# Kernel optimization log

Measured on AMD Instinct MI355X. Metric: run time of the kernel, lower is better.

Reference implementation:

```python
import jax, jax.numpy as jnp
import numpy as np

ALPHA = 16.0  # init kwarg alpha
K = 32        # init kwarg k: threshold = (K+1)-th smallest candidate pair
N, D = 4096, 128
NUM_CLASSES = 512


def setup_inputs() -> dict:
    key = jax.random.key(0)
    k1, k2 = jax.random.split(key)
    x = jax.random.normal(k1, (N, D), dtype=jnp.float32)
    # L2-normalize so self-similarity == 1 (the torch code's `pos_pair_ < 1`
    # filter relies on this to drop the self pair)
    inputs = x / jnp.linalg.norm(x, axis=1, keepdims=True)
    targets = jax.random.randint(k2, (N,), 0, NUM_CLASSES)
    return {"inputs": inputs, "targets": targets}


def reference(inputs, targets):
    sim = inputs @ inputs.T                       # [n, n]
    same = targets[:, None] == targets[None, :]   # [n, n]
    valid_pos = same & (sim < 1.0)                # pos pairs, self excluded
    valid_neg = ~same
    included = valid_pos | valid_neg              # union = torch's `pair`
    inf = jnp.float32(jnp.inf)

    # threshold = sorted(pair)[K] per row (K-th index, 0-based)
    masked = jnp.where(included, sim, inf)
    threshold = jnp.sort(masked, axis=1)[:, K]    # [n]

    base = jnp.mean(sim, axis=1, keepdims=True)   # [n, 1] torch: mean(sim_mat[i])
    w = jnp.exp(ALPHA * (base - sim))             # [n, n]

    below = sim < threshold[:, None]
    pos_sel = valid_pos & below
    neg_sel = valid_neg & below
    pos_sum = jnp.sum(jnp.where(pos_sel, w, 0.0), axis=1)  # [n]
    neg_sum = jnp.sum(jnp.where(neg_sel, w, 0.0), axis=1)  # [n]

    # fallback: if no pos pair below threshold, use the smallest pos similarity
    min_pos = jnp.min(jnp.where(valid_pos, sim, inf), axis=1)
    pos_fallback = jnp.exp(ALPHA * (base[:, 0] - min_pos))
    has_pos = jnp.any(pos_sel, axis=1)
    pos_logit = jnp.where(has_pos, pos_sum, pos_fallback)

    loss = jnp.mean(-jnp.log(pos_logit / (pos_logit + neg_sum)))

    # diagnostics from the LAST row (torch reads pos_pair_/neg_pair_ after loop)
    last = sim[-1]
    mean_pos_sim = jnp.sum(jnp.where(valid_pos[-1], last, 0.0)) / jnp.sum(valid_pos[-1])
    mean_neg_sim = jnp.sum(jnp.where(valid_neg[-1], last, 0.0)) / jnp.sum(valid_neg[-1])
    prec = jnp.float32(0.0)  # torch code: c stays 0
    return loss, prec, mean_pos_sim, mean_neg_sim
```

## Files before the change

kernel.cpp:

```cpp
#include <hip/hip_runtime.h>
#include <math.h>

#define NN 4096
#define DD 128
#define ALPHA_C 16.0f
#define KSEL 32
#define P2F -0.19f
#define SLOTS 16

typedef __attribute__((ext_vector_type(8))) short bf16x8;
typedef __attribute__((ext_vector_type(4))) float f32x4;

__device__ __forceinline__ unsigned f2k(float f) {
  unsigned b = __float_as_uint(f);
  return (b & 0x80000000u) ? ~b : (b | 0x80000000u);
}
__device__ __forceinline__ float k2f(unsigned k) {
  unsigned b = (k & 0x80000000u) ? (k & 0x7FFFFFFFu) : ~k;
  return __uint_as_float(b);
}

__device__ __forceinline__ double wsum_d(double v) {
  #pragma unroll
  for (int m = 32; m; m >>= 1) v += __shfl_xor(v, m, 64);
  return v;
}
__device__ __forceinline__ int wsum_i(int v) {
  #pragma unroll
  for (int m = 32; m; m >>= 1) v += __shfl_xor(v, m, 64);
  return v;
}
__device__ __forceinline__ float wsum_f(float v) {
  #pragma unroll
  for (int m = 32; m; m >>= 1) v += __shfl_xor(v, m, 64);
  return v;
}
__device__ __forceinline__ float wmin_f(float v) {
  #pragma unroll
  for (int m = 32; m; m >>= 1) v = fminf(v, __shfl_xor(v, m, 64));
  return v;
}

__global__ __launch_bounds__(256) void nca_prep(
    const float* __restrict__ x, short* __restrict__ xhi, short* __restrict__ xlo,
    double* __restrict__ selfdot, int* __restrict__ flag) {
  __shared__ double sd[16][16];

  const int tid = threadIdx.x;
  const int f  = blockIdx.x * 256 + tid;
  if (f == 0) flag[0] = 0;
  const int l  = f & 63;
  const int kb = (f >> 6) & 3;
  const int rg = f >> 8;
  const int rloc = l & 15;
  const int row = (rg << 4) + rloc;
  const int k0  = (kb << 5) + ((l >> 4) << 3);
  const float* src = x + (size_t)row * DD + k0;
  float4 v0 = *reinterpret_cast<const float4*>(src);
  float4 v1 = *reinterpret_cast<const float4*>(src + 4);
  float vv[8] = {v0.x, v0.y, v0.z, v0.w, v1.x, v1.y, v1.z, v1.w};
  bf16x8 h, lo;
  double sdp = 0.0;
  #pragma unroll
  for (int q = 0; q < 8; ++q) {
    sdp += (double)vv[q] * (double)vv[q];
    unsigned u  = __float_as_uint(vv[q]);
    unsigned hb = (u + 0x7FFFu + ((u >> 16) & 1u)) >> 16;
    float hf    = __uint_as_float(hb << 16);
    float lf    = vv[q] - hf;
    unsigned ul = __float_as_uint(lf);
    unsigned lb = (ul + 0x7FFFu + ((ul >> 16) & 1u)) >> 16;
    h[q] = (short)hb; lo[q] = (short)lb;
  }
  *reinterpret_cast<bf16x8*>(xhi + (size_t)f * 8) = h;
  *reinterpret_cast<bf16x8*>(xlo + (size_t)f * 8) = lo;

  sd[rloc][(tid >> 4)] = sdp;
  __syncthreads();
  if (tid < 16) {
    double s = 0.0;
    #pragma unroll
    for (int q = 0; q < 16; ++q) s += sd[tid][q];
    selfdot[(rg << 4) + tid] = s;
  }
}

__global__ __launch_bounds__(256) void nca_gemm(
    const short* __restrict__ xhi, const short* __restrict__ xlo,
    const int* __restrict__ tgt, uint2* __restrict__ winbuf,
    unsigned char* __restrict__ wcbuf, float* __restrict__ diagneg) {
  __shared__ int wcl[32];

  const int tid = threadIdx.x;
  const int w   = tid >> 6;
  const int l   = tid & 63;
  const int bid = blockIdx.x;
  const int swz = ((bid & 7) << 8) + (bid >> 3);
  const int rg  = swz >> 4;
  const int cg  = swz & 15;
  const int R   = rg << 5;
  const int C   = (cg << 8) + (w << 6);
  const int rga = rg << 1;
  const int rgb = (cg << 4) + (w << 2);

  if (tid < 32) wcl[tid] = 0;
  __syncthreads();

  f32x4 acc[2][4];
  #pragma unroll
  for (int rt = 0; rt < 2; ++rt)
    #pragma unroll
    for (int t = 0; t < 4; ++t) acc[rt][t] = (f32x4){0.f, 0.f, 0.f, 0.f};

  #pragma unroll
  for (int kb = 0; kb < 4; ++kb) {
    bf16x8 ah[2], al[2], bh[4], bl[4];
    #pragma unroll
    for (int rt = 0; rt < 2; ++rt) {
      const size_t off = ((size_t)((rga + rt) * 4 + kb) * 64 + l) * 8;
      ah[rt] = *reinterpret_cast<const bf16x8*>(xhi + off);
      al[rt] = *reinterpret_cast<const bf16x8*>(xlo + off);
    }
    #pragma unroll
    for (int t = 0; t < 4; ++t) {
      const size_t off = ((size_t)((rgb + t) * 4 + kb) * 64 + l) * 8;
      bh[t] = *reinterpret_cast<const bf16x8*>(xhi + off);
      bl[t] = *reinterpret_cast<const bf16x8*>(xlo + off);
    }
    #pragma unroll
    for (int rt = 0; rt < 2; ++rt)
      #pragma unroll
      for (int t = 0; t < 4; ++t) {
        acc[rt][t] = __builtin_amdgcn_mfma_f32_16x16x32_bf16(ah[rt], bh[t], acc[rt][t], 0, 0, 0);
        acc[rt][t] = __builtin_amdgcn_mfma_f32_16x16x32_bf16(ah[rt], bl[t], acc[rt][t], 0, 0, 0);
        acc[rt][t] = __builtin_amdgcn_mfma_f32_16x16x32_bf16(al[rt], bh[t], acc[rt][t], 0, 0, 0);
      }
  }

  const int rbase = (l >> 4) << 2;
  const int cc    = l & 15;
  const unsigned P2k = f2k(P2F);
  const bool diagblk = (R + 32 == NN);

  int tr[2][4], tc[4];
  #pragma unroll
  for (int rt = 0; rt < 2; ++rt)
    #pragma unroll
    for (int r = 0; r < 4; ++r) tr[rt][r] = tgt[R + (rt << 4) + rbase + r];
  #pragma unroll
  for (int t = 0; t < 4; ++t) tc[t] = tgt[C + (t << 4) + cc];

  #pragma unroll
  for (int rt = 0; rt < 2; ++rt) {
    #pragma unroll
    for (int r = 0; r < 4; ++r) {
      const int row_l = (rt << 4) + rbase + r;
      const int grow  = R + row_l;
      #pragma unroll
      for (int t = 0; t < 4; ++t) {
        const float s = acc[rt][t][r];
        const int j = C + (t << 4) + cc;
        const bool same = (tc[t] == tr[rt][r]);
        const unsigned key = f2k(s);
        const bool app = (j != grow) && (same || (key < P2k));
        if (app) {
          int slot = atomicAdd(&wcl[row_l], 1);
          if (slot < SLOTS)
            winbuf[(size_t)grow * 256 + (cg << 4) + slot] =
                make_uint2(key, same ? 1u : 0u);
        }
      }
    }
  }

  if (diagblk) {
    const int tN1 = tgt[NN - 1];
    float negs = 0.f;
    #pragma unroll
    for (int t = 0; t < 4; ++t)
      negs += (tc[t] != tN1) ? acc[1][t][3] : 0.f;
    negs = ((l >> 4) == 3) ? negs : 0.f;
    #pragma unroll
    for (int m = 1; m < 16; m <<= 1) negs += __shfl_xor(negs, m, 64);
    if (l == 48) diagneg[(cg << 2) + w] = negs;
  }

  __syncthreads();
  if (tid < 32) {
    int c = wcl[tid];
    wcbuf[(size_t)(R + tid) * 16 + cg] = (unsigned char)(c > 255 ? 255 : c);
  }
}

__global__ __launch_bounds__(256) void nca_combine(
    const double* __restrict__ selfdot, const int* __restrict__ tgt,
    const uint2* __restrict__ winbuf, const unsigned char* __restrict__ wcbuf,
    const float* __restrict__ diagneg, int* __restrict__ flag,
    float* __restrict__ row_loss, float* __restrict__ out) {
  const int tid = threadIdx.x, w = tid >> 6, lane = tid & 63;
  const int i = blockIdx.x * 4 + w;

  const double selfd = selfdot[i];
  const bool self_pos = (selfd < 1.0);

  const int wcq_l = (lane < 16) ? (int)wcbuf[(size_t)i * 16 + lane] : 0;
  const bool ovf = (__ballot(wcq_l > SLOTS) != 0ull);

  unsigned k[4]  = {0xFFFFFFFFu, 0xFFFFFFFFu, 0xFFFFFFFFu, 0xFFFFFFFFu};
  unsigned sm[4] = {0u, 0u, 0u, 0u};
  #pragma unroll
  for (int q = 0; q < 4; ++q) {
    const int sigma = (q << 6) + lane;
    const int wcq = __shfl(wcq_l, sigma >> 4, 64);
    if ((sigma & 15) < (wcq < SLOTS ? wcq : SLOTS)) {
      uint2 e = winbuf[(size_t)i * 256 + sigma];
      k[q] = e.x; sm[q] = e.y;
    }
  }

  const unsigned P2k = f2k(P2F);
  int c2 = 0;
  #pragma unroll
  for (int q = 0; q < 4; ++q) c2 += (int)__popcll(__ballot(k[q] < P2k));
  const bool fast = (c2 > KSEL) && (!ovf);
  if (!fast) {
    if (lane == 0) { int p = atomicAdd(&flag[0], 1); flag[1 + p] = i; }
    return;
  }

  unsigned thrkey = 0;
  for (int b = 31; b >= 0; --b) {
    unsigned mid = thrkey | (1u << b);
    int c = 0;
    #pragma unroll
    for (int q = 0; q < 4; ++q) c += (int)__popcll(__ballot(k[q] < mid));
    if (c <= KSEL) thrkey = mid;
  }

  float wp = 0.f, wn = 0.f, minp = __builtin_inff();
  int hp = 0;
  #pragma unroll
  for (int q = 0; q < 4; ++q) {
    const float s = k2f(k[q]);
    if (k[q] < thrkey) {
      float e = expf(-ALPHA_C * s);
      if (sm[q]) { wp += e; hp = 1; } else wn += e;
    }
    if (sm[q] && s < 1.0f) minp = fminf(minp, s);
  }
  wp = wsum_f(wp); wn = wsum_f(wn); hp = wsum_i(hp); minp = wmin_f(minp);

  const float minp2 = self_pos ? fminf(minp, (float)selfd) : minp;
  const float pl = hp ? wp : expf(-ALPHA_C * minp2);
  const float nl = wn;
  if (lane == 0) row_loss[i] = -logf(pl / (pl + nl));

  if (i == NN - 1) {
    float ps = 0.f; int pc = 0;
    #pragma unroll
    for (int q = 0; q < 4; ++q) {
      const float s = k2f(k[q]);
      if (sm[q] && s < 1.0f) { ps += s; pc++; }
    }
    ps = wsum_f(ps); pc = wsum_i(pc);
    float ns = wsum_f(diagneg[lane]);
    const int ti = tgt[NN - 1];
    int nc = 0;
    #pragma unroll
    for (int kk = 0; kk < 16; ++kk) {
      int4 t4 = *reinterpret_cast<const int4*>(tgt + (kk << 8) + (lane << 2));
      nc += (t4.x != ti) + (t4.y != ti) + (t4.z != ti) + (t4.w != ti);
    }
    nc = wsum_i(nc);
    if (lane == 0) {
      out[2] = (ps + (self_pos ? (float)selfd : 0.f)) /
               (float)(pc + (self_pos ? 1 : 0));
      out[3] = ns / (float)nc;
    }
  }
}

__global__ __launch_bounds__(256) void nca_fallback(
    const float* __restrict__ x, const int* __restrict__ tgt,
    const int* __restrict__ flag, float* __restrict__ row_loss,
    float* __restrict__ out) {
  __shared__ float xi[DD];
  __shared__ double redD[4];
  __shared__ int redI[2][4];
  __shared__ double redP[4], redN[4];
  __shared__ float redM[4];
  __shared__ int redH[4], redC[4], redC2[4];
  __shared__ unsigned cbuf[64];
  __shared__ int ccount;

  const int nf = flag[0];
  if (blockIdx.x >= nf) return;
  const int tid = threadIdx.x, w = tid >> 6, lane = tid & 63;
  const int i = flag[1 + blockIdx.x];
  const int ti = tgt[i];
  if (tid < DD) xi[tid] = x[(size_t)i * DD + tid];
  __syncthreads();

  float sims[16];
  const float4* xiv = reinterpret_cast<const float4*>(xi);
  for (int c = 0; c < 16; ++c) {
    const int j = (c << 8) + tid;
    const float4* xj = reinterpret_cast<const float4*>(x + (size_t)j * DD);
    float a0 = 0, a1 = 0, a2 = 0, a3 = 0;
    #pragma unroll
    for (int d = 0; d < 32; ++d) {
      float4 u = xiv[d]; float4 v = xj[d];
      a0 = fmaf(u.x, v.x, a0); a1 = fmaf(u.y, v.y, a1);
      a2 = fmaf(u.z, v.z, a2); a3 = fmaf(u.w, v.w, a3);
    }
    sims[c] = (a0 + a1) + (a2 + a3);
  }

  double sx0 = (double)xi[lane], sx1 = (double)xi[lane + 64];
  const double selfd = wsum_d(sx0 * sx0 + sx1 * sx1);
  const bool self_pos = (selfd < 1.0);

  unsigned kv[16];
  double bs = 0.0;
  #pragma unroll
  for (int c = 0; c < 16; ++c) { bs += (double)sims[c]; kv[c] = f2k(sims[c]); }
  if (!self_pos && ((i & 255) == tid)) kv[i >> 8] = 0xFFFFFFFFu;

  bs = wsum_d(bs);
  if (lane == 0) redD[w] = bs;
  __syncthreads();
  const float basef = (float)((redD[0] + redD[1] + redD[2] + redD[3]) * (1.0 / NN));

  unsigned lo = 0;
  int nLo = 0, nHi = NN, b = 31, par = 0;
  while (b >= 0 && (nHi - nLo) > 64) {
    unsigned mid = lo | (1u << b);
    int c = 0;
    #pragma unroll
    for (int t = 0; t < 16; ++t) c += (kv[t] < mid) ? 1 : 0;
    c = wsum_i(c);
    if (lane == 0) redI[par][w] = c;
    __syncthreads();
    c = redI[par][0] + redI[par][1] + redI[par][2] + redI[par][3];
    par ^= 1;
    if (c <= KSEL) { lo = mid; nLo = c; }
    else nHi = c;
    --b;
  }
  unsigned keysel;
  if ((nHi - nLo) <= 64) {
    const int shift = b + 1;
    const unsigned pfx = lo >> shift;
    if (tid == 0) ccount = 0;
    __syncthreads();
    #pragma unroll
    for (int t = 0; t < 16; ++t)
      if ((kv[t] >> shift) == pfx) { int p = atomicAdd(&ccount, 1); cbuf[p] = kv[t]; }
    __syncthreads();
    const int total = ccount;
    unsigned v = cbuf[lane];
    unsigned long long amask = (total >= 64) ? ~0ull : ((1ull << total) - 1ull);
    int ww = KSEL - nLo;
    for (int bb = b; bb >= 0; --bb) {
      unsigned long long z = __ballot(((amask >> lane) & 1ull) &&
                                      (((v >> bb) & 1u) == 0u));
      int zc = __popcll(z);
      if (ww < zc) amask = z;
      else { ww -= zc; amask &= ~z; }
    }
    int first = __ffsll((unsigned long long)amask) - 1;
    keysel = __shfl(v, first, 64);
  } else {
    keysel = lo;
  }
  const float thr = k2f(keysel);

  double psum = 0.0, nsum = 0.0;
  float minp = __builtin_inff();
  int hasp = 0;
  double pss = 0.0, nss = 0.0;
  int pct = 0, nct = 0;
  #pragma unroll
  for (int c = 0; c < 16; ++c) {
    const int j = (c << 8) + tid;
    const float s = k2f(kv[c]);
    const bool same = (tgt[j] == ti);
    const bool vpos = same && ((j == i) ? self_pos : (s < 1.0f));
    if (vpos) { minp = fminf(minp, s); pss += (double)s; pct++; }
    if (!same) { nss += (double)s; nct++; }
    if (s < thr) {
      float wgt = expf(ALPHA_C * (basef - s));
      if (vpos) { psum += (double)wgt; hasp = 1; }
      else if (!same) nsum += (double)wgt;
    }
  }
  psum = wsum_d(psum); nsum = wsum_d(nsum);
  minp = wmin_f(minp); hasp = wsum_i(hasp);
  if (lane == 0) { redP[w] = psum; redN[w] = nsum; redM[w] = minp; redH[w] = hasp; }
  __syncthreads();
  const double tpsum = redP[0] + redP[1] + redP[2] + redP[3];
  const double tnsum = redN[0] + redN[1] + redN[2] + redN[3];
  const float  tminp = fminf(fminf(redM[0], redM[1]), fminf(redM[2], redM[3]));
  const int    thasp = redH[0] + redH[1] + redH[2] + redH[3];

  if (i == NN - 1) {
    __syncthreads();
    pss = wsum_d(pss); nss = wsum_d(nss);
    pct = wsum_i(pct); nct = wsum_i(nct);
    if (lane == 0) { redP[w] = pss; redN[w] = nss; redC[w] = pct; redC2[w] = nct; }
    __syncthreads();
    if (tid == 0) {
      out[2] = (float)((redP[0] + redP[1] + redP[2] + redP[3]) /
                       (double)(redC[0] + redC[1] + redC[2] + redC[3]));
      out[3] = (float)((redN[0] + redN[1] + redN[2] + redN[3]) /
                       (double)(redC2[0] + redC2[1] + redC2[2] + redC2[3]));
    }
  }
  if (tid == 0) {
    float pl = (thasp > 0) ? (float)tpsum : expf(ALPHA_C * (basef - tminp));
    row_loss[i] = -logf(pl / (pl + (float)tnsum));
  }
}

__global__ void nca_final(const float* __restrict__ row_loss, float* __restrict__ out) {
  __shared__ double redd[4];
  int tid = threadIdx.x;
  double s = 0.0;
  for (int i = tid; i < NN; i += 256) s += (double)row_loss[i];
  #pragma unroll
  for (int m = 32; m; m >>= 1) s += __shfl_xor(s, m, 64);
  if ((tid & 63) == 0) redd[tid >> 6] = s;
  __syncthreads();
  if (tid == 0) {
    double tot = redd[0] + redd[1] + redd[2] + redd[3];
    out[0] = (float)(tot * (1.0 / NN));
    out[1] = 0.0f;
  }
}

extern "C" void kernel_launch(void* const* d_in, const int* in_sizes, int n_in,
                              void* d_out, int out_size, void* d_ws, size_t ws_size,
                              hipStream_t stream) {
  const float* x  = (const float*)d_in[0];
  const int* tgt  = (const int*)d_in[1];
  float* out      = (float*)d_out;

  short* xhi      = (short*)d_ws;
  short* xlo      = xhi + (size_t)NN * DD;
  float* row_loss = (float*)(xlo + (size_t)NN * DD);
  double* selfdot = (double*)(row_loss + NN);
  uint2* winbuf   = (uint2*)(selfdot + NN);
  unsigned char* wcbuf = (unsigned char*)(winbuf + (size_t)NN * 256);
  float* diagneg  = (float*)(wcbuf + (size_t)NN * 16);
  int* flag       = (int*)(diagneg + 64);

  nca_prep<<<NN / 16, 256, 0, stream>>>(x, xhi, xlo, selfdot, flag);
  nca_gemm<<<(NN / 32) * (NN / 256), 256, 0, stream>>>(xhi, xlo, tgt, winbuf, wcbuf, diagneg);
  nca_combine<<<NN / 4, 256, 0, stream>>>(selfdot, tgt, winbuf, wcbuf, diagneg, flag, row_loss, out);
  nca_fallback<<<NN, 256, 0, stream>>>(x, tgt, flag, row_loss, out);
  nca_final<<<1, 256, 0, stream>>>(row_loss, out);
}
```

Measured before the change: 47.54 us.

## Fuse prep, GEMM and combine into one cooperative kernel with grid syncs

Merges the prep, GEMM and combine stages into a single cooperative kernel of 1024 blocks separated by grid-wide barriers. Each block runs two GEMM tiles. The split kernels stay as a fallback when occupancy is too low for a cooperative launch. The fallback kernel now uses a grid-stride loop over 256 blocks instead of launching 4096 mostly-idle blocks. The aim is to cut kernel launch gaps and empty-block scheduling cost, at the price of grid-sync overhead and lower parallelism in the GEMM phase.

New measurement: 47.16 us, median of 2. About the same (-0.8%).

```diff
diff --git a/kernel.cpp b/kernel.cpp
--- a/kernel.cpp
+++ b/kernel.cpp
@@ -1,5 +1,8 @@
 #include <hip/hip_runtime.h>
+#include <hip/hip_cooperative_groups.h>
 #include <math.h>
+
+namespace cg = cooperative_groups;
 
 #define NN 4096
 #define DD 128
@@ -41,13 +44,12 @@
   return v;
 }
 
-__global__ __launch_bounds__(256) void nca_prep(
-    const float* __restrict__ x, short* __restrict__ xhi, short* __restrict__ xlo,
-    double* __restrict__ selfdot, int* __restrict__ flag) {
-  __shared__ double sd[16][16];
-
-  const int tid = threadIdx.x;
-  const int f  = blockIdx.x * 256 + tid;
+
+__device__ __forceinline__ void prep_body(
+    int bid, int tid, const float* __restrict__ x, short* __restrict__ xhi,
+    short* __restrict__ xlo, double* __restrict__ selfdot, int* __restrict__ flag,
+    double (*sd)[16]) {
+  const int f  = bid * 256 + tid;
   if (f == 0) flag[0] = 0;
   const int l  = f & 63;
   const int kb = (f >> 6) & 3;
@@ -83,19 +85,16 @@
     for (int q = 0; q < 16; ++q) s += sd[tid][q];
     selfdot[(rg << 4) + tid] = s;
   }
-}
-
-__global__ __launch_bounds__(256) void nca_gemm(
-    const short* __restrict__ xhi, const short* __restrict__ xlo,
+  __syncthreads();
+}
+
+__device__ __forceinline__ void gemm_body(
+    int vb, int tid, const short* __restrict__ xhi, const short* __restrict__ xlo,
     const int* __restrict__ tgt, uint2* __restrict__ winbuf,
-    unsigned char* __restrict__ wcbuf, float* __restrict__ diagneg) {
-  __shared__ int wcl[32];
-
-  const int tid = threadIdx.x;
+    unsigned char* __restrict__ wcbuf, float* __restrict__ diagneg, int* wcl) {
   const int w   = tid >> 6;
   const int l   = tid & 63;
-  const int bid = blockIdx.x;
-  const int swz = ((bid & 7) << 8) + (bid >> 3);
+  const int swz = ((vb & 7) << 8) + (vb >> 3);
   const int rg  = swz >> 4;
   const int cg  = swz & 15;
   const int R   = rg << 5;
@@ -190,15 +189,17 @@
     int c = wcl[tid];
     wcbuf[(size_t)(R + tid) * 16 + cg] = (unsigned char)(c > 255 ? 255 : c);
   }
-}
-
-__global__ __launch_bounds__(256) void nca_combine(
-    const double* __restrict__ selfdot, const int* __restrict__ tgt,
-    const uint2* __restrict__ winbuf, const unsigned char* __restrict__ wcbuf,
-    const float* __restrict__ diagneg, int* __restrict__ flag,
-    float* __restrict__ row_loss, float* __restrict__ out) {
-  const int tid = threadIdx.x, w = tid >> 6, lane = tid & 63;
-  const int i = blockIdx.x * 4 + w;
+  __syncthreads();
+}
+
+__device__ __forceinline__ void combine_body(
+    int bid, int tid, const double* __restrict__ selfdot,
+    const int* __restrict__ tgt, const uint2* __restrict__ winbuf,
+    const unsigned char* __restrict__ wcbuf, const float* __restrict__ diagneg,
+    int* __restrict__ flag, float* __restrict__ row_loss,
+    float* __restrict__ out) {
+  const int w = tid >> 6, lane = tid & 63;
+  const int i = bid * 4 + w;
 
   const double selfd = selfdot[i];
   const bool self_pos = (selfd < 1.0);
@@ -278,6 +279,54 @@
       out[3] = ns / (float)nc;
     }
   }
+}
+
+__global__ __launch_bounds__(256) void nca_fused(
+    const float* __restrict__ x, const int* __restrict__ tgt,
+    short* __restrict__ xhi, short* __restrict__ xlo,
+    double* __restrict__ selfdot, uint2* __restrict__ winbuf,
+    unsigned char* __restrict__ wcbuf, float* __restrict__ diagneg,
+    int* __restrict__ flag, float* __restrict__ row_loss,
+    float* __restrict__ out) {
+  __shared__ double sd[16][16];
+  __shared__ int wcl[32];
+  cg::grid_group grid = cg::this_grid();
+  const int tid = threadIdx.x;
+  const int bid = blockIdx.x;
+
+  if (bid < 256) prep_body(bid, tid, x, xhi, xlo, selfdot, flag, sd);
+  __threadfence();
+  grid.sync();
+
+  #pragma unroll
+  for (int j = 0; j < 2; ++j)
+    gemm_body(bid * 2 + j, tid, xhi, xlo, tgt, winbuf, wcbuf, diagneg, wcl);
+  __threadfence();
+  grid.sync();
+
+  combine_body(bid, tid, selfdot, tgt, winbuf, wcbuf, diagneg, flag, row_loss, out);
+}
+
+__global__ __launch_bounds__(256) void nca_prep_k(
+    const float* __restrict__ x, short* __restrict__ xhi, short* __restrict__ xlo,
+    double* __restrict__ selfdot, int* __restrict__ flag) {
+  __shared__ double sd[16][16];
+  prep_body(blockIdx.x, threadIdx.x, x, xhi, xlo, selfdot, flag, sd);
+}
+__global__ __launch_bounds__(256) void nca_gemm_k(
+    const short* __restrict__ xhi, const short* __restrict__ xlo,
+    const int* __restrict__ tgt, uint2* __restrict__ winbuf,
+    unsigned char* __restrict__ wcbuf, float* __restrict__ diagneg) {
+  __shared__ int wcl[32];
+  gemm_body(blockIdx.x, threadIdx.x, xhi, xlo, tgt, winbuf, wcbuf, diagneg, wcl);
+}
+__global__ __launch_bounds__(256) void nca_combine_k(
+    const double* __restrict__ selfdot, const int* __restrict__ tgt,
+    const uint2* __restrict__ winbuf, const unsigned char* __restrict__ wcbuf,
+    const float* __restrict__ diagneg, int* __restrict__ flag,
+    float* __restrict__ row_loss, float* __restrict__ out) {
+  combine_body(blockIdx.x, threadIdx.x, selfdot, tgt, winbuf, wcbuf, diagneg,
+               flag, row_loss, out);
 }
 
 __global__ __launch_bounds__(256) void nca_fallback(
@@ -294,131 +343,133 @@
   __shared__ int ccount;
 
   const int nf = flag[0];
-  if (blockIdx.x >= nf) return;
   const int tid = threadIdx.x, w = tid >> 6, lane = tid & 63;
-  const int i = flag[1 + blockIdx.x];
-  const int ti = tgt[i];
-  if (tid < DD) xi[tid] = x[(size_t)i * DD + tid];
-  __syncthreads();
-
-  float sims[16];
-  const float4* xiv = reinterpret_cast<const float4*>(xi);
-  for (int c = 0; c < 16; ++c) {
-    const int j = (c << 8) + tid;
-    const float4* xj = reinterpret_cast<const float4*>(x + (size_t)j * DD);
-    float a0 = 0, a1 = 0, a2 = 0, a3 = 0;
-    #pragma unroll
-    for (int d = 0; d < 32; ++d) {
-      float4 u = xiv[d]; float4 v = xj[d];
-      a0 = fmaf(u.x, v.x, a0); a1 = fmaf(u.y, v.y, a1);
-      a2 = fmaf(u.z, v.z, a2); a3 = fmaf(u.w, v.w, a3);
-    }
-    sims[c] = (a0 + a1) + (a2 + a3);
-  }
-
-  double sx0 = (double)xi[lane], sx1 = (double)xi[lane + 64];
-  const double selfd = wsum_d(sx0 * sx0 + sx1 * sx1);
-  const bool self_pos = (selfd < 1.0);
-
-  unsigned kv[16];
-  double bs = 0.0;
-  #pragma unroll
-  for (int c = 0; c < 16; ++c) { bs += (double)sims[c]; kv[c] = f2k(sims[c]); }
-  if (!self_pos && ((i & 255) == tid)) kv[i >> 8] = 0xFFFFFFFFu;
-
-  bs = wsum_d(bs);
-  if (lane == 0) redD[w] = bs;
-  __syncthreads();
-  const float basef = (float)((redD[0] + redD[1] + redD[2] + redD[3]) * (1.0 / NN));
-
-  unsigned lo = 0;
-  int nLo = 0, nHi = NN, b = 31, par = 0;
-  while (b >= 0 && (nHi - nLo) > 64) {
-    unsigned mid = lo | (1u << b);
-    int c = 0;
-    #pragma unroll
-    for (int t = 0; t < 16; ++t) c += (kv[t] < mid) ? 1 : 0;
-    c = wsum_i(c);
-    if (lane == 0) redI[par][w] = c;
+  for (int fi = blockIdx.x; fi < nf; fi += (int)gridDim.x) {
     __syncthreads();
-    c = redI[par][0] + redI[par][1] + redI[par][2] + redI[par][3];
-    par ^= 1;
-    if (c <= KSEL) { lo = mid; nLo = c; }
-    else nHi = c;
-    --b;
-  }
-  unsigned keysel;
-  if ((nHi - nLo) <= 64) {
-    const int shift = b + 1;
-    const unsigned pfx = lo >> shift;
-    if (tid == 0) ccount = 0;
+    const int i = flag[1 + fi];
+    const int ti = tgt[i];
+    if (tid < DD) xi[tid] = x[(size_t)i * DD + tid];
     __syncthreads();
-    #pragma unroll
-    for (int t = 0; t < 16; ++t)
-      if ((kv[t] >> shift) == pfx) { int p = atomicAdd(&ccount, 1); cbuf[p] = kv[t]; }
+
+    float sims[16];
+    const float4* xiv = reinterpret_cast<const float4*>(xi);
+    for (int c = 0; c < 16; ++c) {
+      const int j = (c << 8) + tid;
+      const float4* xj = reinterpret_cast<const float4*>(x + (size_t)j * DD);
+      float a0 = 0, a1 = 0, a2 = 0, a3 = 0;
+      #pragma unroll
+      for (int d = 0; d < 32; ++d) {
+        float4 u = xiv[d]; float4 v = xj[d];
+        a0 = fmaf(u.x, v.x, a0); a1 = fmaf(u.y, v.y, a1);
+        a2 = fmaf(u.z, v.z, a2); a3 = fmaf(u.w, v.w, a3);
+      }
+      sims[c] = (a0 + a1) + (a2 + a3);
+    }
+
+    double sx0 = (double)xi[lane], sx1 = (double)xi[lane + 64];
+    const double selfd = wsum_d(sx0 * sx0 + sx1 * sx1);
+    const bool self_pos = (selfd < 1.0);
+
+    unsigned kv[16];
+    double bs = 0.0;
+    #pragma unroll
+    for (int c = 0; c < 16; ++c) { bs += (double)sims[c]; kv[c] = f2k(sims[c]); }
+    if (!self_pos && ((i & 255) == tid)) kv[i >> 8] = 0xFFFFFFFFu;
+
+    bs = wsum_d(bs);
+    if (lane == 0) redD[w] = bs;
     __syncthreads();
-    const int total = ccount;
-    unsigned v = cbuf[lane];
-    unsigned long long amask = (total >= 64) ? ~0ull : ((1ull << total) - 1ull);
-    int ww = KSEL - nLo;
-    for (int bb = b; bb >= 0; --bb) {
-      unsigned long long z = __ballot(((amask >> lane) & 1ull) &&
-                                      (((v >> bb) & 1u) == 0u));
-      int zc = __popcll(z);
-      if (ww < zc) amask = z;
-      else { ww -= zc; amask &= ~z; }
-    }
-    int first = __ffsll((unsigned long long)amask) - 1;
-    keysel = __shfl(v, first, 64);
-  } else {
-    keysel = lo;
-  }
-  const float thr = k2f(keysel);
-
-  double psum = 0.0, nsum = 0.0;
-  float minp = __builtin_inff();
-  int hasp = 0;
-  double pss = 0.0, nss = 0.0;
-  int pct = 0, nct = 0;
-  #pragma unroll
-  for (int c = 0; c < 16; ++c) {
-    const int j = (c << 8) + tid;
-    const float s = k2f(kv[c]);
-    const bool same = (tgt[j] == ti);
-    const bool vpos = same && ((j == i) ? self_pos : (s < 1.0f));
-    if (vpos) { minp = fminf(minp, s); pss += (double)s; pct++; }
-    if (!same) { nss += (double)s; nct++; }
-    if (s < thr) {
-      float wgt = expf(ALPHA_C * (basef - s));
-      if (vpos) { psum += (double)wgt; hasp = 1; }
-      else if (!same) nsum += (double)wgt;
-    }
-  }
-  psum = wsum_d(psum); nsum = wsum_d(nsum);
-  minp = wmin_f(minp); hasp = wsum_i(hasp);
-  if (lane == 0) { redP[w] = psum; redN[w] = nsum; redM[w] = minp; redH[w] = hasp; }
-  __syncthreads();
-  const double tpsum = redP[0] + redP[1] + redP[2] + redP[3];
-  const double tnsum = redN[0] + redN[1] + redN[2] + redN[3];
-  const float  tminp = fminf(fminf(redM[0], redM[1]), fminf(redM[2], redM[3]));
-  const int    thasp = redH[0] + redH[1] + redH[2] + redH[3];
-
-  if (i == NN - 1) {
+    const float basef = (float)((redD[0] + redD[1] + redD[2] + redD[3]) * (1.0 / NN));
+
+    unsigned lo = 0;
+    int nLo = 0, nHi = NN, b = 31, par = 0;
+    while (b >= 0 && (nHi - nLo) > 64) {
+      unsigned mid = lo | (1u << b);
+      int c = 0;
+      #pragma unroll
+      for (int t = 0; t < 16; ++t) c += (kv[t] < mid) ? 1 : 0;
+      c = wsum_i(c);
+      if (lane == 0) redI[par][w] = c;
+      __syncthreads();
+      c = redI[par][0] + redI[par][1] + redI[par][2] + redI[par][3];
+      par ^= 1;
+      if (c <= KSEL) { lo = mid; nLo = c; }
+      else nHi = c;
+      --b;
+    }
+    unsigned keysel;
+    if ((nHi - nLo) <= 64) {
+      const int shift = b + 1;
+      const unsigned pfx = lo >> shift;
+      if (tid == 0) ccount = 0;
+      __syncthreads();
+      #pragma unroll
+      for (int t = 0; t < 16; ++t)
+        if ((kv[t] >> shift) == pfx) { int p = atomicAdd(&ccount, 1); cbuf[p] = kv[t]; }
+      __syncthreads();
+      const int total = ccount;
+      unsigned v = cbuf[lane];
+      unsigned long long amask = (total >= 64) ? ~0ull : ((1ull << total) - 1ull);
+      int ww = KSEL - nLo;
+      for (int bb = b; bb >= 0; --bb) {
+        unsigned long long z = __ballot(((amask >> lane) & 1ull) &&
+                                        (((v >> bb) & 1u) == 0u));
+        int zc = __popcll(z);
+        if (ww < zc) amask = z;
+        else { ww -= zc; amask &= ~z; }
+      }
+      int first = __ffsll((unsigned long long)amask) - 1;
+      keysel = __shfl(v, first, 64);
+    } else {
+      keysel = lo;
+    }
+    const float thr = k2f(keysel);
+
+    double psum = 0.0, nsum = 0.0;
+    float minp = __builtin_inff();
+    int hasp = 0;
+    double pss = 0.0, nss = 0.0;
+    int pct = 0, nct = 0;
+    #pragma unroll
+    for (int c = 0; c < 16; ++c) {
+      const int j = (c << 8) + tid;
+      const float s = k2f(kv[c]);
+      const bool same = (tgt[j] == ti);
+      const bool vpos = same && ((j == i) ? self_pos : (s < 1.0f));
+      if (vpos) { minp = fminf(minp, s); pss += (double)s; pct++; }
+      if (!same) { nss += (double)s; nct++; }
+      if (s < thr) {
+        float wgt = expf(ALPHA_C * (basef - s));
+        if (vpos) { psum += (double)wgt; hasp = 1; }
+        else if (!same) nsum += (double)wgt;
+      }
+    }
+    psum = wsum_d(psum); nsum = wsum_d(nsum);
+    minp = wmin_f(minp); hasp = wsum_i(hasp);
+    if (lane == 0) { redP[w] = psum; redN[w] = nsum; redM[w] = minp; redH[w] = hasp; }
     __syncthreads();
-    pss = wsum_d(pss); nss = wsum_d(nss);
-    pct = wsum_i(pct); nct = wsum_i(nct);
-    if (lane == 0) { redP[w] = pss; redN[w] = nss; redC[w] = pct; redC2[w] = nct; }
-    __syncthreads();
+    const double tpsum = redP[0] + redP[1] + redP[2] + redP[3];
+    const double tnsum = redN[0] + redN[1] + redN[2] + redN[3];
+    const float  tminp = fminf(fminf(redM[0], redM[1]), fminf(redM[2], redM[3]));
+    const int    thasp = redH[0] + redH[1] + redH[2] + redH[3];
+
+    if (i == NN - 1) {
+      __syncthreads();
+      pss = wsum_d(pss); nss = wsum_d(nss);
+      pct = wsum_i(pct); nct = wsum_i(nct);
+      if (lane == 0) { redP[w] = pss; redN[w] = nss; redC[w] = pct; redC2[w] = nct; }
+      __syncthreads();
+      if (tid == 0) {
+        out[2] = (float)((redP[0] + redP[1] + redP[2] + redP[3]) /
+                         (double)(redC[0] + redC[1] + redC[2] + redC[3]));
+        out[3] = (float)((redN[0] + redN[1] + redN[2] + redN[3]) /
+                         (double)(redC2[0] + redC2[1] + redC2[2] + redC2[3]));
+      }
+    }
     if (tid == 0) {
-      out[2] = (float)((redP[0] + redP[1] + redP[2] + redP[3]) /
-                       (double)(redC[0] + redC[1] + redC[2] + redC[3]));
-      out[3] = (float)((redN[0] + redN[1] + redN[2] + redN[3]) /
-                       (double)(redC2[0] + redC2[1] + redC2[2] + redC2[3]));
-    }
-  }
-  if (tid == 0) {
-    float pl = (thasp > 0) ? (float)tpsum : expf(ALPHA_C * (basef - tminp));
-    row_loss[i] = -logf(pl / (pl + (float)tnsum));
+      float pl = (thasp > 0) ? (float)tpsum : expf(ALPHA_C * (basef - tminp));
+      row_loss[i] = -logf(pl / (pl + (float)tnsum));
+    }
   }
 }
 
@@ -454,9 +505,25 @@
   float* diagneg  = (float*)(wcbuf + (size_t)NN * 16);
   int* flag       = (int*)(diagneg + 64);
 
-  nca_prep<<<NN / 16, 256, 0, stream>>>(x, xhi, xlo, selfdot, flag);
-  nca_gemm<<<(NN / 32) * (NN / 256), 256, 0, stream>>>(xhi, xlo, tgt, winbuf, wcbuf, diagneg);
-  nca_combine<<<NN / 4, 256, 0, stream>>>(selfdot, tgt, winbuf, wcbuf, diagneg, flag, row_loss, out);
-  nca_fallback<<<NN, 256, 0, stream>>>(x, tgt, flag, row_loss, out);
+  int maxb = 0;
+  hipError_t oe = hipOccupancyMaxActiveBlocksPerMultiprocessor(
+      &maxb, (const void*)nca_fused, 256, 0);
+  const bool coop = (oe == hipSuccess) && (maxb >= 4);
+
+  if (coop) {
+    void* args[] = {(void*)&x, (void*)&tgt, (void*)&xhi, (void*)&xlo,
+                    (void*)&selfdot, (void*)&winbuf, (void*)&wcbuf,
+                    (void*)&diagneg, (void*)&flag, (void*)&row_loss,
+                    (void*)&out};
+    hipLaunchCooperativeKernel((const void*)nca_fused, dim3(1024), dim3(256),
+                               args, 0, stream);
+  } else {
+    nca_prep_k<<<NN / 16, 256, 0, stream>>>(x, xhi, xlo, selfdot, flag);
+    nca_gemm_k<<<(NN / 32) * (NN / 256), 256, 0, stream>>>(xhi, xlo, tgt,
+                                                           winbuf, wcbuf, diagneg);
+    nca_combine_k<<<NN / 4, 256, 0, stream>>>(selfdot, tgt, winbuf, wcbuf,
+                                              diagneg, flag, row_loss, out);
+  }
+  nca_fallback<<<256, 256, 0, stream>>>(x, tgt, flag, row_loss, out);
   nca_final<<<1, 256, 0, stream>>>(row_loss, out);
 }
```

## Exploit Gram-matrix symmetry: compute upper-triangle tiles and mirror candidates to transposed rows

Applied to the files above, without the earlier changes.

The GEMM now launches only upper-triangular block tiles (1088 instead of 2048). Off-diagonal tiles also scatter their candidate keys into the transposed rows' buffers, using a second per-column counter and separate mirror slot regions. The combine kernel reads the wider per-row candidate layout (768 slots, 12 per lane) and merges the normal and mirrored count buffers. The diagonal-negative diagnostics are rebuilt from mirrored tiles. The fallback kernel becomes a grid-stride loop over 256 blocks instead of one block per row. This roughly halves the MFMA work but adds shared-memory atomics, scattered writes and more combine-side work per row.

New measurement: 57.69 us. +21.4%, slower.

```diff
diff --git a/kernel.cpp b/kernel.cpp
--- a/kernel.cpp
+++ b/kernel.cpp
@@ -6,7 +6,10 @@
 #define ALPHA_C 16.0f
 #define KSEL 32
 #define P2F -0.19f
-#define SLOTS 16
+#define NCAP 48
+#define MCAP 6
+#define GSTR 48
+#define RSLOT 768
 
 typedef __attribute__((ext_vector_type(8))) short bf16x8;
 typedef __attribute__((ext_vector_type(4))) float f32x4;
@@ -43,12 +46,14 @@
 
 __global__ __launch_bounds__(256) void nca_prep(
     const float* __restrict__ x, short* __restrict__ xhi, short* __restrict__ xlo,
-    double* __restrict__ selfdot, int* __restrict__ flag) {
+    double* __restrict__ selfdot, float* __restrict__ diagneg,
+    int* __restrict__ flag) {
   __shared__ double sd[16][16];
 
   const int tid = threadIdx.x;
   const int f  = blockIdx.x * 256 + tid;
   if (f == 0) flag[0] = 0;
+  if (blockIdx.x == 0 && tid < 136) diagneg[tid] = 0.f;
   const int l  = f & 63;
   const int kb = (f >> 6) & 3;
   const int rg = f >> 8;
@@ -88,22 +93,31 @@
 __global__ __launch_bounds__(256) void nca_gemm(
     const short* __restrict__ xhi, const short* __restrict__ xlo,
     const int* __restrict__ tgt, uint2* __restrict__ winbuf,
-    unsigned char* __restrict__ wcbuf, float* __restrict__ diagneg) {
+    unsigned char* __restrict__ wcbufN, unsigned char* __restrict__ wcbufM,
+    float* __restrict__ diagneg) {
   __shared__ int wcl[32];
+  __shared__ int wcl2[256];
 
   const int tid = threadIdx.x;
   const int w   = tid >> 6;
   const int l   = tid & 63;
   const int bid = blockIdx.x;
-  const int swz = ((bid & 7) << 8) + (bid >> 3);
-  const int rg  = swz >> 4;
-  const int cg  = swz & 15;
+  const int swz = (bid & 7) * 136 + (bid >> 3);
+  int tp = swz >> 3;
+  const int s8 = swz & 7;
+  int P = 0;
+  while (tp >= 16 - P) { tp -= 16 - P; ++P; }
+  const int Q  = P + tp;
+  const int rg = (P << 3) + s8;
+  const int cg = Q;
+  const bool MIR = (P != Q);
   const int R   = rg << 5;
   const int C   = (cg << 8) + (w << 6);
   const int rga = rg << 1;
   const int rgb = (cg << 4) + (w << 2);
 
   if (tid < 32) wcl[tid] = 0;
+  wcl2[tid] = 0;
   __syncthreads();
 
   f32x4 acc[2][4];
@@ -140,7 +154,7 @@
   const int rbase = (l >> 4) << 2;
   const int cc    = l & 15;
   const unsigned P2k = f2k(P2F);
-  const bool diagblk = (R + 32 == NN);
+  const int tN1 = (cg == 15) ? tgt[NN - 1] : 0;
 
   int tr[2][4], tc[4];
   #pragma unroll
@@ -165,63 +179,114 @@
         const bool app = (j != grow) && (same || (key < P2k));
         if (app) {
           int slot = atomicAdd(&wcl[row_l], 1);
-          if (slot < SLOTS)
-            winbuf[(size_t)grow * 256 + (cg << 4) + slot] =
+          if (slot < NCAP)
+            winbuf[(size_t)grow * RSLOT + cg * GSTR + slot] =
                 make_uint2(key, same ? 1u : 0u);
+          if (MIR) {
+            const int idx = j - (cg << 8);
+            int m = atomicAdd(&wcl2[idx], 1);
+            if (m < MCAP)
+              winbuf[(size_t)j * RSLOT + P * GSTR + s8 * MCAP + m] =
+                  make_uint2(key, same ? 1u : 0u);
+          }
         }
       }
     }
   }
 
-  if (diagblk) {
-    const int tN1 = tgt[NN - 1];
+  if (cg == 15 && rg == 127) {
     float negs = 0.f;
     #pragma unroll
-    for (int t = 0; t < 4; ++t)
-      negs += (tc[t] != tN1) ? acc[1][t][3] : 0.f;
+    for (int t = 0; t < 4; ++t) negs += (tc[t] != tN1) ? acc[1][t][3] : 0.f;
     negs = ((l >> 4) == 3) ? negs : 0.f;
     #pragma unroll
     for (int m = 1; m < 16; m <<= 1) negs += __shfl_xor(negs, m, 64);
-    if (l == 48) diagneg[(cg << 2) + w] = negs;
+    if (l == 48) diagneg[128 + w] = negs;
+  }
+  if (cg == 15 && MIR && w == 3) {
+    float nm = 0.f;
+    if (cc == 15) {
+      #pragma unroll
+      for (int rt = 0; rt < 2; ++rt)
+        #pragma unroll
+        for (int r = 0; r < 4; ++r)
+          nm += (tr[rt][r] != tN1) ? acc[rt][3][r] : 0.f;
+    }
+    nm += __shfl_xor(nm, 16, 64);
+    nm += __shfl_xor(nm, 32, 64);
+    if (l == 63) diagneg[rg] = nm;
   }
 
   __syncthreads();
   if (tid < 32) {
     int c = wcl[tid];
-    wcbuf[(size_t)(R + tid) * 16 + cg] = (unsigned char)(c > 255 ? 255 : c);
+    wcbufN[(size_t)(R + tid) * 16 + cg] = (unsigned char)(c > 255 ? 255 : c);
+  }
+  if (MIR) {
+    int c = wcl2[tid];
+    wcbufM[(size_t)((cg << 8) + tid) * 128 + (P << 3) + s8] =
+        (unsigned char)(c > 255 ? 255 : c);
   }
 }
 
 __global__ __launch_bounds__(256) void nca_combine(
     const double* __restrict__ selfdot, const int* __restrict__ tgt,
-    const uint2* __restrict__ winbuf, const unsigned char* __restrict__ wcbuf,
-    const float* __restrict__ diagneg, int* __restrict__ flag,
-    float* __restrict__ row_loss, float* __restrict__ out) {
+    const uint2* __restrict__ winbuf, const unsigned char* __restrict__ wcbufN,
+    const unsigned char* __restrict__ wcbufM, const float* __restrict__ diagneg,
+    int* __restrict__ flag, float* __restrict__ row_loss,
+    float* __restrict__ out) {
   const int tid = threadIdx.x, w = tid >> 6, lane = tid & 63;
   const int i = blockIdx.x * 4 + w;
+  const int G = i >> 8;
 
   const double selfd = selfdot[i];
   const bool self_pos = (selfd < 1.0);
 
-  const int wcq_l = (lane < 16) ? (int)wcbuf[(size_t)i * 16 + lane] : 0;
-  const bool ovf = (__ballot(wcq_l > SLOTS) != 0ull);
-
-  unsigned k[4]  = {0xFFFFFFFFu, 0xFFFFFFFFu, 0xFFFFFFFFu, 0xFFFFFFFFu};
-  unsigned sm[4] = {0u, 0u, 0u, 0u};
-  #pragma unroll
-  for (int q = 0; q < 4; ++q) {
+  const int wcN_l = (lane < 16) ? (int)wcbufN[(size_t)i * 16 + lane] : 0;
+  unsigned long long wcM_l = 0;
+  if (lane < 16)
+    wcM_l = reinterpret_cast<const unsigned long long*>(
+        wcbufM + (size_t)i * 128)[lane];
+
+  bool ov = (lane < 16) && (lane >= G) && (wcN_l > NCAP);
+  if (lane < 16 && lane < G) {
+    #pragma unroll
+    for (int b = 0; b < 8; ++b)
+      ov |= (((wcM_l >> (b * 8)) & 255ull) > (unsigned long long)MCAP);
+  }
+  const bool ovf = (__ballot(ov) != 0ull);
+
+  unsigned k[12];
+  int smask = 0;
+  #pragma unroll
+  for (int q = 0; q < 12; ++q) k[q] = 0xFFFFFFFFu;
+  #pragma unroll
+  for (int q = 0; q < 12; ++q) {
     const int sigma = (q << 6) + lane;
-    const int wcq = __shfl(wcq_l, sigma >> 4, 64);
-    if ((sigma & 15) < (wcq < SLOTS ? wcq : SLOTS)) {
-      uint2 e = winbuf[(size_t)i * 256 + sigma];
-      k[q] = e.x; sm[q] = e.y;
+    const int grp  = sigma / GSTR;
+    const int slot = sigma - grp * GSTR;
+    const int cN = __shfl(wcN_l, grp, 64);
+    const unsigned long long mM = __shfl(wcM_l, grp, 64);
+    bool valid;
+    if (grp >= G) {
+      valid = slot < cN;
+    } else {
+      const int sub = slot / MCAP;
+      const int within = slot - sub * MCAP;
+      const int cM = (int)((mM >> (sub * 8)) & 255ull);
+      valid = within < (cM < MCAP ? cM : MCAP);
+    }
+    if (valid) {
+      uint2 e = winbuf[(size_t)i * RSLOT + sigma];
+      k[q] = e.x;
+      smask |= (int)e.y << q;
     }
   }
 
   const unsigned P2k = f2k(P2F);
   int c2 = 0;
   #pragma unroll
-  for (int q = 0; q < 4; ++q) c2 += (int)__popcll(__ballot(k[q] < P2k));
+  for (int q = 0; q < 12; ++q) c2 += (int)__popcll(__ballot(k[q] < P2k));
   const bool fast = (c2 > KSEL) && (!ovf);
   if (!fast) {
     if (lane == 0) { int p = atomicAdd(&flag[0], 1); flag[1 + p] = i; }
@@ -233,20 +298,21 @@
     unsigned mid = thrkey | (1u << b);
     int c = 0;
     #pragma unroll
-    for (int q = 0; q < 4; ++q) c += (int)__popcll(__ballot(k[q] < mid));
+    for (int q = 0; q < 12; ++q) c += (int)__popcll(__ballot(k[q] < mid));
     if (c <= KSEL) thrkey = mid;
   }
 
   float wp = 0.f, wn = 0.f, minp = __builtin_inff();
   int hp = 0;
   #pragma unroll
-  for (int q = 0; q < 4; ++q) {
+  for (int q = 0; q < 12; ++q) {
     const float s = k2f(k[q]);
+    const bool sq = (smask >> q) & 1;
     if (k[q] < thrkey) {
       float e = expf(-ALPHA_C * s);
-      if (sm[q]) { wp += e; hp = 1; } else wn += e;
-    }
-    if (sm[q] && s < 1.0f) minp = fminf(minp, s);
+      if (sq) { wp += e; hp = 1; } else wn += e;
+    }
+    if (sq && s < 1.0f) minp = fminf(minp, s);
   }
   wp = wsum_f(wp); wn = wsum_f(wn); hp = wsum_i(hp); minp = wmin_f(minp);
 
@@ -258,12 +324,14 @@
   if (i == NN - 1) {
     float ps = 0.f; int pc = 0;
     #pragma unroll
-    for (int q = 0; q < 4; ++q) {
+    for (int q = 0; q < 12; ++q) {
       const float s = k2f(k[q]);
-      if (sm[q] && s < 1.0f) { ps += s; pc++; }
+      if (((smask >> q) & 1) && s < 1.0f) { ps += s; pc++; }
     }
     ps = wsum_f(ps); pc = wsum_i(pc);
-    float ns = wsum_f(diagneg[lane]);
+    float ns = 0.f;
+    for (int idx = lane; idx < 136; idx += 64) ns += diagneg[idx];
+    ns = wsum_f(ns);
     const int ti = tgt[NN - 1];
     int nc = 0;
     #pragma unroll
@@ -294,131 +362,133 @@
   __shared__ int ccount;
 
   const int nf = flag[0];
-  if (blockIdx.x >= nf) return;
   const int tid = threadIdx.x, w = tid >> 6, lane = tid & 63;
-  const int i = flag[1 + blockIdx.x];
-  const int ti = tgt[i];
-  if (tid < DD) xi[tid] = x[(size_t)i * DD + tid];
-  __syncthreads();
-
-  float sims[16];
-  const float4* xiv = reinterpret_cast<const float4*>(xi);
-  for (int c = 0; c < 16; ++c) {
-    const int j = (c << 8) + tid;
-    const float4* xj = reinterpret_cast<const float4*>(x + (size_t)j * DD);
-    float a0 = 0, a1 = 0, a2 = 0, a3 = 0;
-    #pragma unroll
-    for (int d = 0; d < 32; ++d) {
-      float4 u = xiv[d]; float4 v = xj[d];
-      a0 = fmaf(u.x, v.x, a0); a1 = fmaf(u.y, v.y, a1);
-      a2 = fmaf(u.z, v.z, a2); a3 = fmaf(u.w, v.w, a3);
-    }
-    sims[c] = (a0 + a1) + (a2 + a3);
-  }
-
-  double sx0 = (double)xi[lane], sx1 = (double)xi[lane + 64];
-  const double selfd = wsum_d(sx0 * sx0 + sx1 * sx1);
-  const bool self_pos = (selfd < 1.0);
-
-  unsigned kv[16];
-  double bs = 0.0;
-  #pragma unroll
-  for (int c = 0; c < 16; ++c) { bs += (double)sims[c]; kv[c] = f2k(sims[c]); }
-  if (!self_pos && ((i & 255) == tid)) kv[i >> 8] = 0xFFFFFFFFu;
-
-  bs = wsum_d(bs);
-  if (lane == 0) redD[w] = bs;
-  __syncthreads();
-  const float basef = (float)((redD[0] + redD[1] + redD[2] + redD[3]) * (1.0 / NN));
-
-  unsigned lo = 0;
-  int nLo = 0, nHi = NN, b = 31, par = 0;
-  while (b >= 0 && (nHi - nLo) > 64) {
-    unsigned mid = lo | (1u << b);
-    int c = 0;
-    #pragma unroll
-    for (int t = 0; t < 16; ++t) c += (kv[t] < mid) ? 1 : 0;
-    c = wsum_i(c);
-    if (lane == 0) redI[par][w] = c;
+  for (int fi = blockIdx.x; fi < nf; fi += (int)gridDim.x) {
     __syncthreads();
-    c = redI[par][0] + redI[par][1] + redI[par][2] + redI[par][3];
-    par ^= 1;
-    if (c <= KSEL) { lo = mid; nLo = c; }
-    else nHi = c;
-    --b;
-  }
-  unsigned keysel;
-  if ((nHi - nLo) <= 64) {
-    const int shift = b + 1;
-    const unsigned pfx = lo >> shift;
-    if (tid == 0) ccount = 0;
+    const int i = flag[1 + fi];
+    const int ti = tgt[i];
+    if (tid < DD) xi[tid] = x[(size_t)i * DD + tid];
     __syncthreads();
-    #pragma unroll
-    for (int t = 0; t < 16; ++t)
-      if ((kv[t] >> shift) == pfx) { int p = atomicAdd(&ccount, 1); cbuf[p] = kv[t]; }
+
+    float sims[16];
+    const float4* xiv = reinterpret_cast<const float4*>(xi);
+    for (int c = 0; c < 16; ++c) {
+      const int j = (c << 8) + tid;
+      const float4* xj = reinterpret_cast<const float4*>(x + (size_t)j * DD);
+      float a0 = 0, a1 = 0, a2 = 0, a3 = 0;
+      #pragma unroll
+      for (int d = 0; d < 32; ++d) {
+        float4 u = xiv[d]; float4 v = xj[d];
+        a0 = fmaf(u.x, v.x, a0); a1 = fmaf(u.y, v.y, a1);
+        a2 = fmaf(u.z, v.z, a2); a3 = fmaf(u.w, v.w, a3);
+      }
+      sims[c] = (a0 + a1) + (a2 + a3);
+    }
+
+    double sx0 = (double)xi[lane], sx1 = (double)xi[lane + 64];
+    const double selfd = wsum_d(sx0 * sx0 + sx1 * sx1);
+    const bool self_pos = (selfd < 1.0);
+
+    unsigned kv[16];
+    double bs = 0.0;
+    #pragma unroll
+    for (int c = 0; c < 16; ++c) { bs += (double)sims[c]; kv[c] = f2k(sims[c]); }
+    if (!self_pos && ((i & 255) == tid)) kv[i >> 8] = 0xFFFFFFFFu;
+
+    bs = wsum_d(bs);
+    if (lane == 0) redD[w] = bs;
     __syncthreads();
-    const int total = ccount;
-    unsigned v = cbuf[lane];
-    unsigned long long amask = (total >= 64) ? ~0ull : ((1ull << total) - 1ull);
-    int ww = KSEL - nLo;
-    for (int bb = b; bb >= 0; --bb) {
-      unsigned long long z = __ballot(((amask >> lane) & 1ull) &&
-                                      (((v >> bb) & 1u) == 0u));
-      int zc = __popcll(z);
-      if (ww < zc) amask = z;
-      else { ww -= zc; amask &= ~z; }
-    }
-    int first = __ffsll((unsigned long long)amask) - 1;
-    keysel = __shfl(v, first, 64);
-  } else {
-    keysel = lo;
-  }
-  const float thr = k2f(keysel);
-
-  double psum = 0.0, nsum = 0.0;
-  float minp = __builtin_inff();
-  int hasp = 0;
-  double pss = 0.0, nss = 0.0;
-  int pct = 0, nct = 0;
-  #pragma unroll
-  for (int c = 0; c < 16; ++c) {
-    const int j = (c << 8) + tid;
-    const float s = k2f(kv[c]);
-    const bool same = (tgt[j] == ti);
-    const bool vpos = same && ((j == i) ? self_pos : (s < 1.0f));
-    if (vpos) { minp = fminf(minp, s); pss += (double)s; pct++; }
-    if (!same) { nss += (double)s; nct++; }
-    if (s < thr) {
-      float wgt = expf(ALPHA_C * (basef - s));
-      if (vpos) { psum += (double)wgt; hasp = 1; }
-      else if (!same) nsum += (double)wgt;
-    }
-  }
-  psum = wsum_d(psum); nsum = wsum_d(nsum);
-  minp = wmin_f(minp); hasp = wsum_i(hasp);
-  if (lane == 0) { redP[w] = psum; redN[w] = nsum; redM[w] = minp; redH[w] = hasp; }
-  __syncthreads();
-  const double tpsum = redP[0] + redP[1] + redP[2] + redP[3];
-  const double tnsum = redN[0] + redN[1] + redN[2] + redN[3];
-  const float  tminp = fminf(fminf(redM[0], redM[1]), fminf(redM[2], redM[3]));
-  const int    thasp = redH[0] + redH[1] + redH[2] + redH[3];
-
-  if (i == NN - 1) {
+    const float basef = (float)((redD[0] + redD[1] + redD[2] + redD[3]) * (1.0 / NN));
+
+    unsigned lo = 0;
+    int nLo = 0, nHi = NN, b = 31, par = 0;
+    while (b >= 0 && (nHi - nLo) > 64) {
+      unsigned mid = lo | (1u << b);
+      int c = 0;
+      #pragma unroll
+      for (int t = 0; t < 16; ++t) c += (kv[t] < mid) ? 1 : 0;
+      c = wsum_i(c);
+      if (lane == 0) redI[par][w] = c;
+      __syncthreads();
+      c = redI[par][0] + redI[par][1] + redI[par][2] + redI[par][3];
+      par ^= 1;
+      if (c <= KSEL) { lo = mid; nLo = c; }
+      else nHi = c;
+      --b;
+    }
+    unsigned keysel;
+    if ((nHi - nLo) <= 64) {
+      const int shift = b + 1;
+      const unsigned pfx = lo >> shift;
+      if (tid == 0) ccount = 0;
+      __syncthreads();
+      #pragma unroll
+      for (int t = 0; t < 16; ++t)
+        if ((kv[t] >> shift) == pfx) { int p = atomicAdd(&ccount, 1); cbuf[p] = kv[t]; }
+      __syncthreads();
+      const int total = ccount;
+      unsigned v = cbuf[lane];
+      unsigned long long amask = (total >= 64) ? ~0ull : ((1ull << total) - 1ull);
+      int ww = KSEL - nLo;
+      for (int bb = b; bb >= 0; --bb) {
+        unsigned long long z = __ballot(((amask >> lane) & 1ull) &&
+                                        (((v >> bb) & 1u) == 0u));
+        int zc = __popcll(z);
+        if (ww < zc) amask = z;
+        else { ww -= zc; amask &= ~z; }
+      }
+      int first = __ffsll((unsigned long long)amask) - 1;
+      keysel = __shfl(v, first, 64);
+    } else {
+      keysel = lo;
+    }
+    const float thr = k2f(keysel);
+
+    double psum = 0.0, nsum = 0.0;
+    float minp = __builtin_inff();
+    int hasp = 0;
+    double pss = 0.0, nss = 0.0;
+    int pct = 0, nct = 0;
+    #pragma unroll
+    for (int c = 0; c < 16; ++c) {
+      const int j = (c << 8) + tid;
+      const float s = k2f(kv[c]);
+      const bool same = (tgt[j] == ti);
+      const bool vpos = same && ((j == i) ? self_pos : (s < 1.0f));
+      if (vpos) { minp = fminf(minp, s); pss += (double)s; pct++; }
+      if (!same) { nss += (double)s; nct++; }
+      if (s < thr) {
+        float wgt = expf(ALPHA_C * (basef - s));
+        if (vpos) { psum += (double)wgt; hasp = 1; }
+        else if (!same) nsum += (double)wgt;
+      }
+    }
+    psum = wsum_d(psum); nsum = wsum_d(nsum);
+    minp = wmin_f(minp); hasp = wsum_i(hasp);
+    if (lane == 0) { redP[w] = psum; redN[w] = nsum; redM[w] = minp; redH[w] = hasp; }
     __syncthreads();
-    pss = wsum_d(pss); nss = wsum_d(nss);
-    pct = wsum_i(pct); nct = wsum_i(nct);
-    if (lane == 0) { redP[w] = pss; redN[w] = nss; redC[w] = pct; redC2[w] = nct; }
-    __syncthreads();
+    const double tpsum = redP[0] + redP[1] + redP[2] + redP[3];
+    const double tnsum = redN[0] + redN[1] + redN[2] + redN[3];
+    const float  tminp = fminf(fminf(redM[0], redM[1]), fminf(redM[2], redM[3]));
+    const int    thasp = redH[0] + redH[1] + redH[2] + redH[3];
+
+    if (i == NN - 1) {
+      __syncthreads();
+      pss = wsum_d(pss); nss = wsum_d(nss);
+      pct = wsum_i(pct); nct = wsum_i(nct);
+      if (lane == 0) { redP[w] = pss; redN[w] = nss; redC[w] = pct; redC2[w] = nct; }
+      __syncthreads();
+      if (tid == 0) {
+        out[2] = (float)((redP[0] + redP[1] + redP[2] + redP[3]) /
+                         (double)(redC[0] + redC[1] + redC[2] + redC[3]));
+        out[3] = (float)((redN[0] + redN[1] + redN[2] + redN[3]) /
+                         (double)(redC2[0] + redC2[1] + redC2[2] + redC2[3]));
+      }
+    }
     if (tid == 0) {
-      out[2] = (float)((redP[0] + redP[1] + redP[2] + redP[3]) /
-                       (double)(redC[0] + redC[1] + redC[2] + redC[3]));
-      out[3] = (float)((redN[0] + redN[1] + redN[2] + redN[3]) /
-                       (double)(redC2[0] + redC2[1] + redC2[2] + redC2[3]));
-    }
-  }
-  if (tid == 0) {
-    float pl = (thasp > 0) ? (float)tpsum : expf(ALPHA_C * (basef - tminp));
-    row_loss[i] = -logf(pl / (pl + (float)tnsum));
+      float pl = (thasp > 0) ? (float)tpsum : expf(ALPHA_C * (basef - tminp));
+      row_loss[i] = -logf(pl / (pl + (float)tnsum));
+    }
   }
 }
 
@@ -450,13 +520,15 @@
   float* row_loss = (float*)(xlo + (size_t)NN * DD);
   double* selfdot = (double*)(row_loss + NN);
   uint2* winbuf   = (uint2*)(selfdot + NN);
-  unsigned char* wcbuf = (unsigned char*)(winbuf + (size_t)NN * 256);
-  float* diagneg  = (float*)(wcbuf + (size_t)NN * 16);
-  int* flag       = (int*)(diagneg + 64);
-
-  nca_prep<<<NN / 16, 256, 0, stream>>>(x, xhi, xlo, selfdot, flag);
-  nca_gemm<<<(NN / 32) * (NN / 256), 256, 0, stream>>>(xhi, xlo, tgt, winbuf, wcbuf, diagneg);
-  nca_combine<<<NN / 4, 256, 0, stream>>>(selfdot, tgt, winbuf, wcbuf, diagneg, flag, row_loss, out);
-  nca_fallback<<<NN, 256, 0, stream>>>(x, tgt, flag, row_loss, out);
+  unsigned char* wcbufN = (unsigned char*)(winbuf + (size_t)NN * RSLOT);
+  unsigned char* wcbufM = wcbufN + (size_t)NN * 16;
+  float* diagneg  = (float*)(wcbufM + (size_t)NN * 128);
+  int* flag       = (int*)(diagneg + 136);
+
+  nca_prep<<<NN / 16, 256, 0, stream>>>(x, xhi, xlo, selfdot, diagneg, flag);
+  nca_gemm<<<1088, 256, 0, stream>>>(xhi, xlo, tgt, winbuf, wcbufN, wcbufM, diagneg);
+  nca_combine<<<NN / 4, 256, 0, stream>>>(selfdot, tgt, winbuf, wcbufN, wcbufM,
+                                          diagneg, flag, row_loss, out);
+  nca_fallback<<<256, 256, 0, stream>>>(x, tgt, flag, row_loss, out);
   nca_final<<<1, 256, 0, stream>>>(row_loss, out);
 }
```
